# Optimization experiments

Measured on AMD Instinct MI355X. Metric: run time of the kernel, lower is better.

Reference implementation:

```python
import jax, jax.numpy as jnp
import numpy as np

N = 32768
L_ENC = 100
L_DEC = 50
H = 100
D_FEAT = L_ENC + 2 * (L_ENC // 2 + 1)  # 202: signal + rfft real + rfft imag


def setup_inputs() -> dict:
    key = jax.random.key(0)
    ks = jax.random.split(key, 11)
    s = 0.05
    return {
        "encoder_input": jax.random.normal(ks[0], (N, L_ENC, 1), dtype=jnp.float32),
        "w_enc": jax.random.normal(ks[1], (H, D_FEAT), dtype=jnp.float32) * s,
        "b_enc": jax.random.normal(ks[2], (H,), dtype=jnp.float32) * s,
        "w_ih": jax.random.normal(ks[3], (3 * H, 1), dtype=jnp.float32) * s,
        "b_ih": jax.random.normal(ks[4], (3 * H,), dtype=jnp.float32) * s,
        "w_hh": jax.random.normal(ks[5], (3 * H, H), dtype=jnp.float32) * s,
        "b_hh": jax.random.normal(ks[6], (3 * H,), dtype=jnp.float32) * s,
        "w1": jax.random.normal(ks[7], (H // 2, H), dtype=jnp.float32) * s,
        "b1": jax.random.normal(ks[8], (H // 2,), dtype=jnp.float32) * s,
        "w2": jax.random.normal(ks[9], (1, H // 2), dtype=jnp.float32) * s,
        "b2": jax.random.normal(ks[10], (1,), dtype=jnp.float32) * s,
    }


def reference(encoder_input, w_enc, b_enc, w_ih, b_ih, w_hh, b_hh, w1, b1, w2, b2):
    sig = encoder_input[:, :, 0]                       # [N, L]
    spec = jnp.fft.rfft(sig, axis=-1)                  # [N, L//2+1] complex
    feat = jnp.concatenate([sig, spec.real.astype(sig.dtype), spec.imag.astype(sig.dtype)], axis=-1)  # [N, 202]
    h0 = jnp.tanh(feat @ w_enc.T + b_enc)              # [N, H] encoder -> initial hidden
    x0 = encoder_input[:, -1, :]                       # [N, 1] last signal value seeds decoder

    def step(carry, _):
        h, x = carry
        gi = x @ w_ih.T + b_ih                         # [N, 3H]
        gh = h @ w_hh.T + b_hh                         # [N, 3H]
        i_r, i_z, i_n = jnp.split(gi, 3, axis=-1)
        h_r, h_z, h_n = jnp.split(gh, 3, axis=-1)
        r = jax.nn.sigmoid(i_r + h_r)
        z = jax.nn.sigmoid(i_z + h_z)
        n = jnp.tanh(i_n + r * h_n)
        h_new = (1.0 - z) * n + z * h                  # GRUCell update
        y = jax.nn.leaky_relu(h_new @ w1.T + b1, 0.01) @ w2.T + b2  # [N, 1]
        x_new = jax.lax.stop_gradient(y)               # matches x.clone().detach()
        return (h_new, x_new), y

    _, ys = jax.lax.scan(step, (h0, x0), None, length=L_DEC)  # ys: [L_dec, N, 1]
    return jnp.transpose(ys, (1, 0, 2))                # [N, L_dec, 1]
```

## Files before the change

kernel.cpp:

```cpp
#include <hip/hip_runtime.h>

typedef __bf16 bf16x8 __attribute__((ext_vector_type(8)));
typedef float f32x4 __attribute__((ext_vector_type(4)));

#define WS_WENC 0
#define WS_WHH  14336
#define WS_W1   57344
#define LOG2E 1.4426950408889634f

__device__ __forceinline__ float fast_exp2(float x) {
#if __has_builtin(__builtin_amdgcn_exp2f)
  return __builtin_amdgcn_exp2f(x);
#else
  return exp2f(x);
#endif
}
__device__ __forceinline__ float fast_rcp(float x) {
#if __has_builtin(__builtin_amdgcn_rcpf)
  return __builtin_amdgcn_rcpf(x);
#else
  return 1.f / x;
#endif
}

__global__ void prep_kernel(const float* __restrict__ w_enc,
                            const float* __restrict__ b_enc,
                            const float* __restrict__ w_hh,
                            const float* __restrict__ b_ih,
                            const float* __restrict__ b_hh,
                            const float* __restrict__ w1,
                            const float* __restrict__ b1,
                            __bf16* __restrict__ ws) {
  int idx = blockIdx.x * 256 + threadIdx.x;
  if (idx < 14336) {
    int i = idx >> 7, n = idx & 127;
    float acc = 0.f;
    if (i < 100) {
      if (n < 100) {
        const float* wr = w_enc + i * 202;
        acc = wr[n];
        #pragma unroll 1
        for (int k = 0; k <= 50; ++k) {
          int m = (k * n) % 100;
          float th = 0.062831853071795864f * (float)m;
          float s, c;
          __sincosf(th, &s, &c);
          acc += wr[100 + k] * c - wr[151 + k] * s;
        }
        acc *= 2.f * LOG2E;
      } else if (n == 100) {
        acc = 2.f * LOG2E * b_enc[i];
      }
    }
    ws[idx] = (__bf16)acc;
  } else if (idx < 57344) {
    int j = idx - 14336;
    int g = j / 14336;
    int rem = j - g * 14336;
    int u2 = rem >> 7, c2 = rem & 127;
    float scale = (g == 2) ? 2.f * LOG2E : LOG2E;
    float v = 0.f;
    if (u2 < 100) {
      if (c2 < 100) v = scale * w_hh[(g * 100 + u2) * 100 + c2];
      else if (c2 == 100) {
        v = (g == 2) ? scale * b_hh[200 + u2]
                     : scale * (b_ih[g * 100 + u2] + b_hh[g * 100 + u2]);
      }
    }
    ws[idx] = (__bf16)v;
  } else if (idx < 65536) {
    int j = idx - 57344;
    int r2 = j >> 7, c2 = j & 127;
    float v = 0.f;
    if (r2 < 50) {
      if (c2 < 100) v = w1[r2 * 100 + c2];
      else if (c2 == 100) v = b1[r2];
    }
    ws[idx] = (__bf16)v;
  }
}

__device__ __forceinline__ f32x4 mfma16(bf16x8 a, bf16x8 b, f32x4 c) {
  return __builtin_amdgcn_mfma_f32_16x16x32_bf16(a, b, c, 0, 0, 0);
}
__device__ __forceinline__ float sigm2(float a) { return fast_rcp(1.f + fast_exp2(-a)); }
__device__ __forceinline__ float tanh2(float b) { return fmaf(2.f, fast_rcp(1.f + fast_exp2(-b)), -1.f); }

__global__ __launch_bounds__(448, 4)
void gru_main(const float* __restrict__ enc,
              const float* __restrict__ w_ih,
              const float* __restrict__ b_ih,
              const float* __restrict__ w2,
              const float* __restrict__ b2,
              const __bf16* __restrict__ ws,
              float* __restrict__ out) {
  __shared__ __align__(16) __bf16 hbuf[2][32 * 136];
  __shared__ __align__(16) __bf16 wYl[64 * 136];
  __shared__ __align__(16) float xq[2][16][4];
  __shared__ __align__(16) float outstage[32 * 52];
  __shared__ float w2l[64];

  const int tid = threadIdx.x;
  const int w = tid >> 6;
  const int l = tid & 63;
  const int c = l & 15;
  const int grp = l >> 4;
  const int klo = 8 * grp;
  const int seqbase = blockIdx.x * 32;
  const int u = 16 * w + c;
  const bool vu = (u < 100);
  const float padf = (u == 100) ? 1.f : 0.f;

  for (int i = tid; i < 2 * 32 * 136; i += 448)
    hbuf[0][i] = (__bf16)((i % 136 == 100) ? 1.f : 0.f);
  for (int i = tid; i < 1024; i += 448) {
    int row = i >> 4, off = (i & 15) * 8;
    *(bf16x8*)&wYl[row * 136 + off] = *(const bf16x8*)(ws + WS_W1 + row * 128 + off);
  }
  if (tid < 64) w2l[tid] = (tid < 50) ? w2[tid] : 0.f;

  float wihr = 0.f, wihz = 0.f, wihn = 0.f, bin_ = 0.f;
  if (vu) {
    wihr = w_ih[u] * LOG2E;
    wihz = w_ih[100 + u] * LOG2E;
    wihn = w_ih[200 + u] * (2.f * LOG2E);
    bin_ = b_ih[200 + u] * (2.f * LOG2E);
  }
  const int ytile = (w < 3) ? w : ((w == 3) ? 3 : (w - 4));
  const int yg0 = (w < 4) ? 0 : 1;
  const bool dual = (w == 3);
  const float b2v = b2[0];

  bf16x8 wR[3][4];
  #pragma unroll
  for (int g = 0; g < 3; ++g) {
    #pragma unroll
    for (int kt = 0; kt < 4; ++kt)
      wR[g][kt] = *(const bf16x8*)(ws + WS_WHH + (g * 112 + u) * 128 + kt * 32 + klo);
  }

  float h_old[2][4];
  {
    #pragma unroll
    for (int g = 0; g < 2; ++g) {
      f32x4 hc = {0.f, 0.f, 0.f, 0.f};
      const float* srow = enc + (size_t)(seqbase + 16 * g + c) * 100;
      #pragma unroll
      for (int kt = 0; kt < 4; ++kt) {
        bf16x8 wE = *(const bf16x8*)(ws + WS_WENC + u * 128 + kt * 32 + klo);
        int t0 = kt * 32 + klo;
        float f0 = 0.f, f1 = 0.f, f2 = 0.f, f3 = 0.f, f4 = 0.f, f5 = 0.f, f6 = 0.f, f7 = 0.f;
        if (t0 + 8 <= 100) {
          float4 va = *(const float4*)(srow + t0);
          float4 vb = *(const float4*)(srow + t0 + 4);
          f0 = va.x; f1 = va.y; f2 = va.z; f3 = va.w;
          f4 = vb.x; f5 = vb.y; f6 = vb.z; f7 = vb.w;
        } else if (t0 < 100) {
          float4 va = *(const float4*)(srow + t0);
          f0 = va.x; f1 = va.y; f2 = va.z; f3 = va.w;
          f4 = 1.f;
        }
        bf16x8 a;
        a[0] = (__bf16)f0; a[1] = (__bf16)f1; a[2] = (__bf16)f2; a[3] = (__bf16)f3;
        a[4] = (__bf16)f4; a[5] = (__bf16)f5; a[6] = (__bf16)f6; a[7] = (__bf16)f7;
        hc = mfma16(a, wE, hc);
      }
      #pragma unroll
      for (int r = 0; r < 4; ++r) h_old[g][r] = vu ? tanh2(hc[r]) : 0.f;
    }
  }

  __syncthreads();
  #pragma unroll
  for (int g = 0; g < 2; ++g)
    #pragma unroll
    for (int r = 0; r < 4; ++r)
      hbuf[0][(16 * g + 4 * grp + r) * 136 + u] = (__bf16)(vu ? h_old[g][r] : padf);
  __syncthreads();

  #pragma unroll 1
  for (int t = 0; t <= 50; ++t) {
    const int rb = t & 1;
    if (t > 0) {
      const int ntask = dual ? 2 : 1;
      #pragma unroll 1
      for (int gi = 0; gi < ntask; ++gi) {
        const int g = dual ? gi : yg0;
        f32x4 Cy = {0.f, 0.f, 0.f, 0.f};
        #pragma unroll
        for (int kt = 0; kt < 4; ++kt) {
          bf16x8 wyf = *(const bf16x8*)&wYl[(ytile * 16 + c) * 136 + kt * 32 + klo];
          bf16x8 ag = *(const bf16x8*)&hbuf[rb][(16 * g + c) * 136 + kt * 32 + klo];
          Cy = mfma16(wyf, ag, Cy);
        }
        float p = 0.f;
        #pragma unroll
        for (int r = 0; r < 4; ++r) {
          float v = Cy[r];
          v = fmaxf(v, 0.01f * v);
          p = fmaf(w2l[ytile * 16 + 4 * grp + r], v, p);
        }
        p += __shfl_xor(p, 16);
        p += __shfl_xor(p, 32);
        if (l < 16) xq[g][l][ytile] = p;
      }
    }
    f32x4 Cr0 = {0.f,0.f,0.f,0.f}, Cz0 = {0.f,0.f,0.f,0.f}, Cn0 = {0.f,0.f,0.f,0.f};
    if (t < 50) {
      #pragma unroll
      for (int kt = 0; kt < 4; ++kt) {
        bf16x8 a = *(const bf16x8*)&hbuf[rb][c * 136 + kt * 32 + klo];
        Cr0 = mfma16(a, wR[0][kt], Cr0);
        Cz0 = mfma16(a, wR[1][kt], Cz0);
        Cn0 = mfma16(a, wR[2][kt], Cn0);
      }
    }
    __syncthreads();

    if (t < 50) {
      const int wb = rb ^ 1;
      f32x4 Cr1 = {0.f,0.f,0.f,0.f}, Cz1 = {0.f,0.f,0.f,0.f}, Cn1 = {0.f,0.f,0.f,0.f};
      #pragma unroll
      for (int kt = 0; kt < 4; ++kt) {
        bf16x8 a = *(const bf16x8*)&hbuf[rb][(16 + c) * 136 + kt * 32 + klo];
        Cr1 = mfma16(a, wR[0][kt], Cr1);
        Cz1 = mfma16(a, wR[1][kt], Cz1);
        Cn1 = mfma16(a, wR[2][kt], Cn1);
      }
      {
        float xv[4];
        if (t > 0) {
          #pragma unroll
          for (int r = 0; r < 4; ++r) {
            float4 xp = *(const float4*)xq[0][4 * grp + r];
            xv[r] = b2v + xp.x + xp.y + xp.z + xp.w;
          }
          if (c == 0 && w == 0) {
            #pragma unroll
            for (int r = 0; r < 4; ++r)
              outstage[(4 * grp + r) * 52 + (t - 1)] = xv[r];
          }
        } else {
          #pragma unroll
          for (int r = 0; r < 4; ++r)
            xv[r] = enc[(size_t)(seqbase + 4 * grp + r) * 100 + 99];
        }
        #pragma unroll
        for (int r = 0; r < 4; ++r) {
          float ar = fmaf(xv[r], wihr, Cr0[r]);
          float rg = sigm2(ar);
          float az = fmaf(xv[r], wihz, Cz0[r]);
          float zg = sigm2(az);
          float bn = fmaf(rg, Cn0[r], fmaf(xv[r], wihn, bin_));
          float ng = tanh2(bn);
          float hn = fmaf(zg, h_old[0][r] - ng, ng);
          h_old[0][r] = hn;
          hbuf[wb][(4 * grp + r) * 136 + u] = (__bf16)(vu ? hn : padf);
        }
      }
      {
        float xv[4];
        if (t > 0) {
          #pragma unroll
          for (int r = 0; r < 4; ++r) {
            float4 xp = *(const float4*)xq[1][4 * grp + r];
            xv[r] = b2v + xp.x + xp.y + xp.z + xp.w;
          }
          if (c == 0 && w == 3) {
            #pragma unroll
            for (int r = 0; r < 4; ++r)
              outstage[(16 + 4 * grp + r) * 52 + (t - 1)] = xv[r];
          }
        } else {
          #pragma unroll
          for (int r = 0; r < 4; ++r)
            xv[r] = enc[(size_t)(seqbase + 16 + 4 * grp + r) * 100 + 99];
        }
        #pragma unroll
        for (int r = 0; r < 4; ++r) {
          float ar = fmaf(xv[r], wihr, Cr1[r]);
          float rg = sigm2(ar);
          float az = fmaf(xv[r], wihz, Cz1[r]);
          float zg = sigm2(az);
          float bn = fmaf(rg, Cn1[r], fmaf(xv[r], wihn, bin_));
          float ng = tanh2(bn);
          float hn = fmaf(zg, h_old[1][r] - ng, ng);
          h_old[1][r] = hn;
          hbuf[wb][(16 + 4 * grp + r) * 136 + u] = (__bf16)(vu ? hn : padf);
        }
      }
    } else {
      #pragma unroll
      for (int g = 0; g < 2; ++g) {
        if (c == 0 && w == 3 * g) {
          #pragma unroll
          for (int r = 0; r < 4; ++r) {
            float4 xp = *(const float4*)xq[g][4 * grp + r];
            outstage[(16 * g + 4 * grp + r) * 52 + (t - 1)] =
                b2v + xp.x + xp.y + xp.z + xp.w;
          }
        }
      }
    }
    __syncthreads();
  }

  for (int i = tid; i < 32 * 50; i += 448) {
    int s = i / 50, tp = i - s * 50;
    out[(size_t)(seqbase + s) * 50 + tp] = outstage[s * 52 + tp];
  }
}

extern "C" void kernel_launch(void* const* d_in, const int* in_sizes, int n_in,
                              void* d_out, int out_size, void* d_ws, size_t ws_size,
                              hipStream_t stream) {
  const float* enc   = (const float*)d_in[0];
  const float* w_enc = (const float*)d_in[1];
  const float* b_enc = (const float*)d_in[2];
  const float* w_ih  = (const float*)d_in[3];
  const float* b_ih  = (const float*)d_in[4];
  const float* w_hh  = (const float*)d_in[5];
  const float* b_hh  = (const float*)d_in[6];
  const float* w1    = (const float*)d_in[7];
  const float* b1    = (const float*)d_in[8];
  const float* w2    = (const float*)d_in[9];
  const float* b2    = (const float*)d_in[10];
  __bf16* ws = (__bf16*)d_ws;
  float* out = (float*)d_out;

  prep_kernel<<<256, 256, 0, stream>>>(w_enc, b_enc, w_hh, b_ih, b_hh, w1, b1, ws);
  gru_main<<<32768 / 32, 448, 0, stream>>>(enc, w_ih, b_ih, w2, b2, ws, out);
}
```

Baseline: 318.8 us.

## Pack two 32-sequence teams into one 896-thread block sharing W1 tile

Doubles the block to 14 waves handling 64 sequences, split into two teams of 7 waves that each own 32 sequences. The W1 shared tile and w2 are loaded once per block instead of once per 32 sequences, and the number of blocks is halved. In exchange, block-wide barriers now couple twice as many waves, and launch bounds change from (448,4) to (896,2), which alters register budget and occupancy granularity.

```diff
diff --git a/kernel.cpp b/kernel.cpp
--- a/kernel.cpp
+++ b/kernel.cpp
@@ -86,7 +86,7 @@
 __device__ __forceinline__ float sigm2(float a) { return fast_rcp(1.f + fast_exp2(-a)); }
 __device__ __forceinline__ float tanh2(float b) { return fmaf(2.f, fast_rcp(1.f + fast_exp2(-b)), -1.f); }
 
-__global__ __launch_bounds__(448, 4)
+__global__ __launch_bounds__(896, 2)
 void gru_main(const float* __restrict__ enc,
               const float* __restrict__ w_ih,
               const float* __restrict__ b_ih,
@@ -94,26 +94,30 @@
               const float* __restrict__ b2,
               const __bf16* __restrict__ ws,
               float* __restrict__ out) {
-  __shared__ __align__(16) __bf16 hbuf[2][32 * 136];
+  __shared__ __align__(16) __bf16 hbuf[2][64 * 136];
   __shared__ __align__(16) __bf16 wYl[64 * 136];
-  __shared__ __align__(16) float xq[2][16][4];
-  __shared__ __align__(16) float outstage[32 * 52];
+  __shared__ __align__(16) float xq[4][16][4];
+  __shared__ __align__(16) float outstage[64 * 52];
   __shared__ float w2l[64];
 
   const int tid = threadIdx.x;
   const int w = tid >> 6;
+  const int T = (w >= 7);
+  const int wt = w - 7 * T;
   const int l = tid & 63;
   const int c = l & 15;
   const int grp = l >> 4;
   const int klo = 8 * grp;
-  const int seqbase = blockIdx.x * 32;
-  const int u = 16 * w + c;
+  const int seqbase = blockIdx.x * 64;
+  const int u = 16 * wt + c;
   const bool vu = (u < 100);
   const float padf = (u == 100) ? 1.f : 0.f;
-
-  for (int i = tid; i < 2 * 32 * 136; i += 448)
+  const int g0 = 2 * T;
+  const int g1 = 2 * T + 1;
+
+  for (int i = tid; i < 2 * 64 * 136; i += 896)
     hbuf[0][i] = (__bf16)((i % 136 == 100) ? 1.f : 0.f);
-  for (int i = tid; i < 1024; i += 448) {
+  for (int i = tid; i < 1024; i += 896) {
     int row = i >> 4, off = (i & 15) * 8;
     *(bf16x8*)&wYl[row * 136 + off] = *(const bf16x8*)(ws + WS_W1 + row * 128 + off);
   }
@@ -126,9 +130,9 @@
     wihn = w_ih[200 + u] * (2.f * LOG2E);
     bin_ = b_ih[200 + u] * (2.f * LOG2E);
   }
-  const int ytile = (w < 3) ? w : ((w == 3) ? 3 : (w - 4));
-  const int yg0 = (w < 4) ? 0 : 1;
-  const bool dual = (w == 3);
+  const int ytile = (wt < 3) ? wt : ((wt == 3) ? 3 : (wt - 4));
+  const int yg = (wt < 4) ? g0 : g1;
+  const bool dual = (wt == 3);
   const float b2v = b2[0];
 
   bf16x8 wR[3][4];
@@ -142,9 +146,9 @@
   float h_old[2][4];
   {
     #pragma unroll
-    for (int g = 0; g < 2; ++g) {
+    for (int gl = 0; gl < 2; ++gl) {
       f32x4 hc = {0.f, 0.f, 0.f, 0.f};
-      const float* srow = enc + (size_t)(seqbase + 16 * g + c) * 100;
+      const float* srow = enc + (size_t)(seqbase + 16 * (g0 + gl) + c) * 100;
       #pragma unroll
       for (int kt = 0; kt < 4; ++kt) {
         bf16x8 wE = *(const bf16x8*)(ws + WS_WENC + u * 128 + kt * 32 + klo);
@@ -166,16 +170,16 @@
         hc = mfma16(a, wE, hc);
       }
       #pragma unroll
-      for (int r = 0; r < 4; ++r) h_old[g][r] = vu ? tanh2(hc[r]) : 0.f;
+      for (int r = 0; r < 4; ++r) h_old[gl][r] = vu ? tanh2(hc[r]) : 0.f;
     }
   }
 
   __syncthreads();
   #pragma unroll
-  for (int g = 0; g < 2; ++g)
+  for (int gl = 0; gl < 2; ++gl)
     #pragma unroll
     for (int r = 0; r < 4; ++r)
-      hbuf[0][(16 * g + 4 * grp + r) * 136 + u] = (__bf16)(vu ? h_old[g][r] : padf);
+      hbuf[0][(16 * (g0 + gl) + 4 * grp + r) * 136 + u] = (__bf16)(vu ? h_old[gl][r] : padf);
   __syncthreads();
 
   #pragma unroll 1
@@ -185,7 +189,7 @@
       const int ntask = dual ? 2 : 1;
       #pragma unroll 1
       for (int gi = 0; gi < ntask; ++gi) {
-        const int g = dual ? gi : yg0;
+        const int g = dual ? (g0 + gi) : yg;
         f32x4 Cy = {0.f, 0.f, 0.f, 0.f};
         #pragma unroll
         for (int kt = 0; kt < 4; ++kt) {
@@ -209,7 +213,7 @@
     if (t < 50) {
       #pragma unroll
       for (int kt = 0; kt < 4; ++kt) {
-        bf16x8 a = *(const bf16x8*)&hbuf[rb][c * 136 + kt * 32 + klo];
+        bf16x8 a = *(const bf16x8*)&hbuf[rb][(16 * g0 + c) * 136 + kt * 32 + klo];
         Cr0 = mfma16(a, wR[0][kt], Cr0);
         Cz0 = mfma16(a, wR[1][kt], Cz0);
         Cn0 = mfma16(a, wR[2][kt], Cn0);
@@ -222,7 +226,7 @@
       f32x4 Cr1 = {0.f,0.f,0.f,0.f}, Cz1 = {0.f,0.f,0.f,0.f}, Cn1 = {0.f,0.f,0.f,0.f};
       #pragma unroll
       for (int kt = 0; kt < 4; ++kt) {
-        bf16x8 a = *(const bf16x8*)&hbuf[rb][(16 + c) * 136 + kt * 32 + klo];
+        bf16x8 a = *(const bf16x8*)&hbuf[rb][(16 * g1 + c) * 136 + kt * 32 + klo];
         Cr1 = mfma16(a, wR[0][kt], Cr1);
         Cz1 = mfma16(a, wR[1][kt], Cz1);
         Cn1 = mfma16(a, wR[2][kt], Cn1);
@@ -232,18 +236,18 @@
         if (t > 0) {
           #pragma unroll
           for (int r = 0; r < 4; ++r) {
-            float4 xp = *(const float4*)xq[0][4 * grp + r];
+            float4 xp = *(const float4*)xq[g0][4 * grp + r];
             xv[r] = b2v + xp.x + xp.y + xp.z + xp.w;
           }
-          if (c == 0 && w == 0) {
+          if (c == 0 && wt == 0) {
             #pragma unroll
             for (int r = 0; r < 4; ++r)
-              outstage[(4 * grp + r) * 52 + (t - 1)] = xv[r];
+              outstage[(16 * g0 + 4 * grp + r) * 52 + (t - 1)] = xv[r];
           }
         } else {
           #pragma unroll
           for (int r = 0; r < 4; ++r)
-            xv[r] = enc[(size_t)(seqbase + 4 * grp + r) * 100 + 99];
+            xv[r] = enc[(size_t)(seqbase + 16 * g0 + 4 * grp + r) * 100 + 99];
         }
         #pragma unroll
         for (int r = 0; r < 4; ++r) {
@@ -255,7 +259,7 @@
           float ng = tanh2(bn);
           float hn = fmaf(zg, h_old[0][r] - ng, ng);
           h_old[0][r] = hn;
-          hbuf[wb][(4 * grp + r) * 136 + u] = (__bf16)(vu ? hn : padf);
+          hbuf[wb][(16 * g0 + 4 * grp + r) * 136 + u] = (__bf16)(vu ? hn : padf);
         }
       }
       {
@@ -263,18 +267,18 @@
         if (t > 0) {
           #pragma unroll
           for (int r = 0; r < 4; ++r) {
-            float4 xp = *(const float4*)xq[1][4 * grp + r];
+            float4 xp = *(const float4*)xq[g1][4 * grp + r];
             xv[r] = b2v + xp.x + xp.y + xp.z + xp.w;
           }
-          if (c == 0 && w == 3) {
+          if (c == 0 && wt == 3) {
             #pragma unroll
             for (int r = 0; r < 4; ++r)
-              outstage[(16 + 4 * grp + r) * 52 + (t - 1)] = xv[r];
+              outstage[(16 * g1 + 4 * grp + r) * 52 + (t - 1)] = xv[r];
           }
         } else {
           #pragma unroll
           for (int r = 0; r < 4; ++r)
-            xv[r] = enc[(size_t)(seqbase + 16 + 4 * grp + r) * 100 + 99];
+            xv[r] = enc[(size_t)(seqbase + 16 * g1 + 4 * grp + r) * 100 + 99];
         }
         #pragma unroll
         for (int r = 0; r < 4; ++r) {
@@ -286,13 +290,14 @@
           float ng = tanh2(bn);
           float hn = fmaf(zg, h_old[1][r] - ng, ng);
           h_old[1][r] = hn;
-          hbuf[wb][(16 + 4 * grp + r) * 136 + u] = (__bf16)(vu ? hn : padf);
+          hbuf[wb][(16 * g1 + 4 * grp + r) * 136 + u] = (__bf16)(vu ? hn : padf);
         }
       }
     } else {
       #pragma unroll
-      for (int g = 0; g < 2; ++g) {
-        if (c == 0 && w == 3 * g) {
+      for (int gl = 0; gl < 2; ++gl) {
+        const int g = g0 + gl;
+        if (c == 0 && wt == 3 * gl) {
           #pragma unroll
           for (int r = 0; r < 4; ++r) {
             float4 xp = *(const float4*)xq[g][4 * grp + r];
@@ -305,7 +310,7 @@
     __syncthreads();
   }
 
-  for (int i = tid; i < 32 * 50; i += 448) {
+  for (int i = tid; i < 64 * 50; i += 896) {
     int s = i / 50, tp = i - s * 50;
     out[(size_t)(seqbase + s) * 50 + tp] = outstage[s * 52 + tp];
   }
@@ -329,5 +334,5 @@
   float* out = (float*)d_out;
 
   prep_kernel<<<256, 256, 0, stream>>>(w_enc, b_enc, w_hh, b_ih, b_hh, w1, b1, ws);
-  gru_main<<<32768 / 32, 448, 0, stream>>>(enc, w_ih, b_ih, w2, b2, ws, out);
-}
+  gru_main<<<32768 / 64, 896, 0, stream>>>(enc, w_ih, b_ih, w2, b2, ws, out);
+}
```

Result: slower. 361.7 us (+13.4%).
